# Kernel tuning notes

Measured on AMD Instinct MI355X. Metric: run time of the kernel, lower is better.

Reference implementation:

```python
import jax, jax.numpy as jnp
import numpy as np

T, B = 2048, 128
H = 128          # hidden_size
QH = 1024        # query_hidden_size
NF = 32          # num_convolution_filters
K = 31           # convolution_filter_size (odd, same padding)


def setup_inputs() -> dict:
    key = jax.random.key(0)
    ks = jax.random.split(key, 10)
    encoded_tokens = jax.random.normal(ks[0], (T, B, H), dtype=jnp.float32)
    tokens_mask = jax.random.randint(ks[1], (B, T), 0, 2).astype(jnp.bool_)
    query = jax.random.normal(ks[2], (1, B, QH), dtype=jnp.float32)
    cumulative_alignment = jax.random.uniform(ks[3], (B, T), dtype=jnp.float32)
    # parameters
    conv_w = jax.random.normal(ks[4], (NF, 1, K), dtype=jnp.float32) * 0.1   # Conv1d weight [out,in,k]
    conv_b = jnp.zeros((NF,), dtype=jnp.float32)
    Wq = jax.random.normal(ks[5], (H, QH), dtype=jnp.float32) * (1.0 / np.sqrt(QH))
    bq = jnp.zeros((H,), dtype=jnp.float32)
    Wa = jax.random.normal(ks[6], (H, NF), dtype=jnp.float32) * (1.0 / np.sqrt(NF))
    ba = jnp.zeros((H,), dtype=jnp.float32)
    score_w = jax.random.normal(ks[7], (H,), dtype=jnp.float32) * (1.0 / np.sqrt(H))  # xavier-ish
    score_b = jnp.zeros((H,), dtype=jnp.float32)
    return dict(encoded_tokens=encoded_tokens, tokens_mask=tokens_mask, query=query,
                cumulative_alignment=cumulative_alignment, conv_w=conv_w, conv_b=conv_b,
                Wq=Wq, bq=bq, Wa=Wa, ba=ba, score_w=score_w, score_b=score_b)


def reference(encoded_tokens, tokens_mask, query, cumulative_alignment,
              conv_w, conv_b, Wq, bq, Wa, ba, score_w, score_b):
    # location features: Conv1d over cumulative alignment, same padding
    loc = jax.lax.conv_general_dilated(
        cumulative_alignment[:, None, :], conv_w,
        window_strides=(1,), padding=[((K - 1) // 2, (K - 1) // 2)],
        dimension_numbers=('NCH', 'OIH', 'NCH'))  # [B, NF, T]
    loc = loc + conv_b[None, :, None]
    loc = jnp.transpose(loc, (2, 0, 1))                        # [T, B, NF]
    loc = jnp.einsum('tbf,hf->tbh', loc, Wa) + ba              # [T, B, H]
    q = jnp.einsum('obq,hq->obh', query, Wq) + bq              # [1, B, H]
    # additive score: tanh of fused elementwise sum, then project to scalar
    score = jnp.tanh(encoded_tokens + q + loc + score_b)       # [T, B, H]
    s = jnp.einsum('tbh,h->bt', score, score_w)                # [B, T]
    s = jnp.where(tokens_mask, -jnp.inf, s)
    alignment = jax.nn.softmax(s, axis=1)                      # [B, T]
    context = jnp.einsum('bt,tbh->bh', alignment, encoded_tokens)  # [B, H]
    cumulative_alignment = cumulative_alignment + alignment
    return context, cumulative_alignment, alignment
```

## Files before the change

### kernel.cpp

```cpp
#include <hip/hip_runtime.h>
#include <stdint.h>

#define T_DIM 2048
#define B_DIM 128
#define H_DIM 128
#define QH_DIM 1024
#define NF 32
#define KW 31
#define TB 128
#define NTILE (T_DIM / TB)
#define CPAD_ROW (T_DIM + 32)

#define PREP_NB 512
#define G_NB 8

#define NEG_INF (-__builtin_inff())

typedef float v2f __attribute__((ext_vector_type(2)));

__device__ __forceinline__ float fast_tanh(float x) {
    float e = __expf(2.0f * x);
    return 1.0f - 2.0f * __builtin_amdgcn_rcpf(1.0f + e);
}

template <int C>
__device__ __forceinline__ float dpp_add(float x) {
    int m = __builtin_amdgcn_update_dpp(0, __float_as_int(x), C, 0xf, 0xf, true);
    return x + __int_as_float(m);
}
__device__ __forceinline__ float wave_sum64(float x) {
    x = dpp_add<0x111>(x); x = dpp_add<0x112>(x); x = dpp_add<0x114>(x); x = dpp_add<0x118>(x);
    x = dpp_add<0x142>(x); x = dpp_add<0x143>(x);
    return __int_as_float(__builtin_amdgcn_readlane(__float_as_int(x), 63));
}

__global__ __launch_bounds__(512)
void kA_prep(const float* __restrict__ cum, const void* __restrict__ mask,
             float* __restrict__ cpad, float* __restrict__ mbias,
             const float* __restrict__ Wa, const float* __restrict__ conv_w,
             float* __restrict__ Gt,
             const float* __restrict__ query, const float* __restrict__ Wq,
             const float* __restrict__ bq, const float* __restrict__ conv_b,
             const float* __restrict__ ba, const float* __restrict__ score_b,
             float* __restrict__ qb) {
    const int bid = blockIdx.x;
    const int tid = threadIdx.x;

    if (bid < PREP_NB) {
        const int gid = bid * 512 + tid;
        const int b = gid >> 11, t = gid & 2047;
        const int l = tid & 63;
        uint32_t u = ((const uint32_t*)mask)[l];
        unsigned long long hi = __ballot(u > 1u);
        unsigned long long nf = __ballot(u != 0u && u != 0x3f800000u);
        int layout = (hi == 0ull) ? 0 : ((nf == 0ull) ? 2 : 1);
        bool m;
        if (layout == 0)      m = ((const int32_t*)mask)[gid] != 0;
        else if (layout == 1) m = ((const uint8_t*)mask)[gid] != 0;
        else                  m = ((const float*)mask)[gid] != 0.0f;
        mbias[gid] = m ? NEG_INF : 0.0f;
        cpad[b * CPAD_ROW + 16 + t] = cum[gid];
        if (t < 16) cpad[b * CPAD_ROW + t] = 0.0f;
        else if (t >= T_DIM - 16) cpad[b * CPAD_ROW + 32 + t] = 0.0f;
    } else if (bid < PREP_NB + G_NB) {
        const int gid = (bid - PREP_NB) * 512 + tid;
        if (gid < KW * H_DIM) {
            const int k = gid >> 7, h = gid & 127;
            float acc = 0.0f;
            #pragma unroll
            for (int f = 0; f < NF; ++f) acc = fmaf(Wa[h * NF + f], conv_w[f * KW + k], acc);
            Gt[gid] = acc;
        }
    } else {
        const int b = bid - (PREP_NB + G_NB);
        const int h = tid & 127, qtr = tid >> 7;
        __shared__ __align__(16) float qrow[QH_DIM];
        __shared__ float partial[512];
        for (int i = tid; i < QH_DIM; i += 512) qrow[i] = query[b * QH_DIM + i];
        __syncthreads();
        const float4* wq4 = (const float4*)(Wq + (size_t)h * QH_DIM + qtr * 256);
        const float4* q4 = (const float4*)(qrow + qtr * 256);
        float acc = 0.0f;
        #pragma unroll 4
        for (int j = 0; j < 64; ++j) {
            float4 w = wq4[j], q = q4[j];
            acc += w.x * q.x + w.y * q.y + w.z * q.z + w.w * q.w;
        }
        if (qtr == 0) {
            float cb = bq[h] + ba[h] + score_b[h];
            #pragma unroll
            for (int f = 0; f < NF; ++f) cb = fmaf(Wa[h * NF + f], conv_b[f], cb);
            acc += cb;
        }
        partial[tid] = acc;
        __syncthreads();
        if (tid < 128)
            qb[b * H_DIM + h] = partial[h] + partial[h + 128] + partial[h + 256] + partial[h + 384];
    }
}

__global__ __launch_bounds__(256, 4)
void k2_fused(const float* __restrict__ enc, const float* __restrict__ cpad,
              const float* __restrict__ mbias, const float* __restrict__ Gt,
              const float* __restrict__ qb, const float* __restrict__ score_w,
              float* __restrict__ s_out, float* __restrict__ o_part,
              float* __restrict__ ml_part) {
    const int b = blockIdx.x;
    const int tl = blockIdx.y;
    const int tid = threadIdx.x;
    const int l = tid & 63;
    const int wv = __builtin_amdgcn_readfirstlane(tid >> 6);
    const int tw0 = tl * TB + wv * 32;

    __shared__ float oc[4][H_DIM];
    __shared__ float mwl[4], lwl[4];

    v2f G[KW];
    #pragma unroll
    for (int k = 0; k < KW; ++k) G[k] = *(const v2f*)(Gt + k * H_DIM + 2 * l);

    const v2f base = *(const v2f*)(qb + b * H_DIM + 2 * l);
    const v2f w2 = *(const v2f*)(score_w + 2 * l);
    const float* crow = cpad + b * CPAD_ROW;
    const float* mrow = mbias + b * T_DIM;

    float m_w = NEG_INF, l_w = 0.0f;
    v2f o = {0.0f, 0.0f};
    float sv = 0.0f;

    #pragma unroll
    for (int c = 0; c < 4; ++c) {
        const int tb = tw0 + c * 8;

        float sc[38];
        #pragma unroll
        for (int j = 0; j < 38; ++j) sc[j] = crow[tb + 1 + j];

        v2f ee[8];
        #pragma unroll
        for (int it = 0; it < 8; ++it)
            ee[it] = *(const v2f*)(enc + ((size_t)(tb + it) * B_DIM + b) * H_DIM + 2 * l);

        float su[8];
        #pragma unroll
        for (int it = 0; it < 8; ++it) {
            v2f acc = base;
            #pragma unroll
            for (int k = 0; k < KW; ++k)
                acc = __builtin_elementwise_fma(G[k], (v2f){sc[it + k], sc[it + k]}, acc);
            const v2f a2 = acc + ee[it];
            float p = w2.x * fast_tanh(a2.x) + w2.y * fast_tanh(a2.y);
            su[it] = wave_sum64(p) + mrow[tb + it];
        }

        #pragma unroll
        for (int it = 0; it < 8; ++it) sv = (l == c * 8 + it) ? su[it] : sv;

        float m8 = su[0];
        #pragma unroll
        for (int it = 1; it < 8; ++it) m8 = fmaxf(m8, su[it]);
        const float m_new = fmaxf(m_w, m8);
        const float m_use = (m_new == NEG_INF) ? 0.0f : m_new;
        const float alpha = __expf(m_w - m_use);
        float lsum = 0.0f;
        v2f osum = {0.0f, 0.0f};
        #pragma unroll
        for (int it = 0; it < 8; ++it) {
            const float e = __expf(su[it] - m_use);
            lsum += e;
            osum = __builtin_elementwise_fma((v2f){e, e}, ee[it], osum);
        }
        l_w = fmaf(l_w, alpha, lsum);
        o = __builtin_elementwise_fma(o, (v2f){alpha, alpha}, osum);
        m_w = m_new;
    }

    if (l < 32) s_out[b * T_DIM + tw0 + l] = sv;

    oc[wv][2 * l] = o.x;
    oc[wv][2 * l + 1] = o.y;
    if (l == 0) { mwl[wv] = m_w; lwl[wv] = l_w; }
    __syncthreads();
    if (tid < H_DIM) {
        const float mb = fmaxf(fmaxf(mwl[0], mwl[1]), fmaxf(mwl[2], mwl[3]));
        const float mu = (mb == NEG_INF) ? 0.0f : mb;
        const float b0 = __expf(mwl[0] - mu), b1 = __expf(mwl[1] - mu);
        const float b2 = __expf(mwl[2] - mu), b3 = __expf(mwl[3] - mu);
        const float ov = oc[0][tid] * b0 + oc[1][tid] * b1 + oc[2][tid] * b2 + oc[3][tid] * b3;
        const int tbase = b * NTILE + tl;
        o_part[tbase * H_DIM + tid] = ov;
        if (tid == 0) {
            ml_part[tbase * 2] = mb;
            ml_part[tbase * 2 + 1] = lwl[0] * b0 + lwl[1] * b1 + lwl[2] * b2 + lwl[3] * b3;
        }
    }
}

__global__ __launch_bounds__(256)
void k5_final(float* __restrict__ s_align, const float* __restrict__ cum_in,
              float* __restrict__ cum_out, const float* __restrict__ o_part,
              const float* __restrict__ ml_part, float* __restrict__ ctx) {
    const int b = blockIdx.x, seg = blockIdx.y, tid = threadIdx.x;
    __shared__ float sm[NTILE], sl[NTILE], sb[NTILE];
    if (tid < NTILE) {
        sm[tid] = ml_part[(b * NTILE + tid) * 2];
        sl[tid] = ml_part[(b * NTILE + tid) * 2 + 1];
    }
    __syncthreads();
    float M = sm[0];
    #pragma unroll
    for (int i = 1; i < NTILE; ++i) M = fmaxf(M, sm[i]);
    const float M_use = (M == NEG_INF) ? 0.0f : M;
    if (tid < NTILE) sb[tid] = __expf(sm[tid] - M_use);
    __syncthreads();
    float L = 0.0f;
    #pragma unroll
    for (int i = 0; i < NTILE; ++i) L = fmaf(sl[i], sb[i], L);
    const float invL = 1.0f / L;
    if (seg == 0 && tid < H_DIM) {
        float ov = 0.0f;
        #pragma unroll
        for (int i = 0; i < NTILE; ++i)
            ov = fmaf(o_part[(b * NTILE + i) * H_DIM + tid], sb[i], ov);
        ctx[b * H_DIM + tid] = ov * invL;
    }
    #pragma unroll
    for (int j = 0; j < 2; ++j) {
        const int idx = b * T_DIM + seg * 512 + tid + j * 256;
        const float a = __expf(s_align[idx] - M_use) * invL;
        s_align[idx] = a;
        cum_out[idx] = cum_in[idx] + a;
    }
}

extern "C" void kernel_launch(void* const* d_in, const int* in_sizes, int n_in,
                              void* d_out, int out_size, void* d_ws, size_t ws_size,
                              hipStream_t stream) {
    const float* enc     = (const float*)d_in[0];
    const void*  mask    = d_in[1];
    const float* query   = (const float*)d_in[2];
    const float* cum     = (const float*)d_in[3];
    const float* conv_w  = (const float*)d_in[4];
    const float* conv_b  = (const float*)d_in[5];
    const float* Wq      = (const float*)d_in[6];
    const float* bq      = (const float*)d_in[7];
    const float* Wa      = (const float*)d_in[8];
    const float* ba      = (const float*)d_in[9];
    const float* score_w = (const float*)d_in[10];
    const float* score_b = (const float*)d_in[11];

    float* ctx_out   = (float*)d_out;
    float* cum_out   = ctx_out + B_DIM * H_DIM;
    float* align_out = cum_out + B_DIM * T_DIM;

    float* Gt     = (float*)d_ws;
    float* qb     = Gt + 4096;
    float* o_part = qb + B_DIM * H_DIM;
    float* ml     = o_part + B_DIM * NTILE * H_DIM;
    float* cpad   = ml + 8192;
    float* mb     = cpad + B_DIM * CPAD_ROW;

    kA_prep<<<PREP_NB + G_NB + B_DIM, 512, 0, stream>>>(
        cum, mask, cpad, mb, Wa, conv_w, Gt,
        query, Wq, bq, conv_b, ba, score_b, qb);
    k2_fused<<<dim3(B_DIM, NTILE), 256, 0, stream>>>(enc, cpad, mb, Gt, qb, score_w,
                                                     align_out, o_part, ml);
    k5_final<<<dim3(B_DIM, 4), 256, 0, stream>>>(align_out, cum, cum_out, o_part, ml, ctx_out);
}
```

Measured before the change: 233.5 us.

## Split query projection across more blocks and double-buffer encoder loads

The query projection in the prep kernel is split into four segment blocks per batch row, each writing a partial result. The fused kernel now sums the four partials when it forms its base vector. The fused kernel also prefetches the next chunk of encoder rows into a double buffer while the current chunk is computed, which is meant to hide global load latency. Launch bounds drop from 4 to 3 blocks per SM to make room for the extra registers, which trades occupancy for software pipelining.

```diff
diff --git a/kernel.cpp b/kernel.cpp
--- a/kernel.cpp
+++ b/kernel.cpp
@@ -13,6 +13,7 @@
 
 #define PREP_NB 512
 #define G_NB 8
+#define QB_SEG 4
 
 #define NEG_INF (-__builtin_inff())
 
@@ -42,7 +43,7 @@
              const float* __restrict__ query, const float* __restrict__ Wq,
              const float* __restrict__ bq, const float* __restrict__ conv_b,
              const float* __restrict__ ba, const float* __restrict__ score_b,
-             float* __restrict__ qb) {
+             float* __restrict__ qb_part) {
     const int bid = blockIdx.x;
     const int tid = threadIdx.x;
 
@@ -72,37 +73,40 @@
             Gt[gid] = acc;
         }
     } else {
-        const int b = bid - (PREP_NB + G_NB);
-        const int h = tid & 127, qtr = tid >> 7;
-        __shared__ __align__(16) float qrow[QH_DIM];
+        const int qbid = bid - (PREP_NB + G_NB);
+        const int b = qbid >> 2, seg = qbid & 3;
+        const int h = tid & 127, sub = tid >> 7;
+        __shared__ __align__(16) float qrow[256];
         __shared__ float partial[512];
-        for (int i = tid; i < QH_DIM; i += 512) qrow[i] = query[b * QH_DIM + i];
+        if (tid < 256) qrow[tid] = query[b * QH_DIM + seg * 256 + tid];
         __syncthreads();
-        const float4* wq4 = (const float4*)(Wq + (size_t)h * QH_DIM + qtr * 256);
-        const float4* q4 = (const float4*)(qrow + qtr * 256);
+        const float4* wq4 = (const float4*)(Wq + (size_t)h * QH_DIM + seg * 256 + sub * 64);
+        const float4* q4 = (const float4*)(qrow + sub * 64);
         float acc = 0.0f;
-        #pragma unroll 4
-        for (int j = 0; j < 64; ++j) {
+        #pragma unroll
+        for (int j = 0; j < 16; ++j) {
             float4 w = wq4[j], q = q4[j];
             acc += w.x * q.x + w.y * q.y + w.z * q.z + w.w * q.w;
         }
-        if (qtr == 0) {
-            float cb = bq[h] + ba[h] + score_b[h];
-            #pragma unroll
-            for (int f = 0; f < NF; ++f) cb = fmaf(Wa[h * NF + f], conv_b[f], cb);
-            acc += cb;
-        }
         partial[tid] = acc;
         __syncthreads();
-        if (tid < 128)
-            qb[b * H_DIM + h] = partial[h] + partial[h + 128] + partial[h + 256] + partial[h + 384];
-    }
-}
-
-__global__ __launch_bounds__(256, 4)
+        if (tid < 128) {
+            float r = partial[h] + partial[h + 128] + partial[h + 256] + partial[h + 384];
+            if (seg == 0) {
+                float cb = bq[h] + ba[h] + score_b[h];
+                #pragma unroll
+                for (int f = 0; f < NF; ++f) cb = fmaf(Wa[h * NF + f], conv_b[f], cb);
+                r += cb;
+            }
+            qb_part[(seg * B_DIM + b) * H_DIM + h] = r;
+        }
+    }
+}
+
+__global__ __launch_bounds__(256, 3)
 void k2_fused(const float* __restrict__ enc, const float* __restrict__ cpad,
               const float* __restrict__ mbias, const float* __restrict__ Gt,
-              const float* __restrict__ qb, const float* __restrict__ score_w,
+              const float* __restrict__ qb_part, const float* __restrict__ score_w,
               float* __restrict__ s_out, float* __restrict__ o_part,
               float* __restrict__ ml_part) {
     const int b = blockIdx.x;
@@ -119,27 +123,40 @@
     #pragma unroll
     for (int k = 0; k < KW; ++k) G[k] = *(const v2f*)(Gt + k * H_DIM + 2 * l);
 
-    const v2f base = *(const v2f*)(qb + b * H_DIM + 2 * l);
+    const float* qp = qb_part + b * H_DIM + 2 * l;
+    v2f base = *(const v2f*)(qp);
+    base += *(const v2f*)(qp + B_DIM * H_DIM);
+    base += *(const v2f*)(qp + 2 * B_DIM * H_DIM);
+    base += *(const v2f*)(qp + 3 * B_DIM * H_DIM);
+
     const v2f w2 = *(const v2f*)(score_w + 2 * l);
     const float* crow = cpad + b * CPAD_ROW;
     const float* mrow = mbias + b * T_DIM;
+    const float* erow = enc + ((size_t)tw0 * B_DIM + b) * H_DIM + 2 * l;
 
     float m_w = NEG_INF, l_w = 0.0f;
     v2f o = {0.0f, 0.0f};
     float sv = 0.0f;
 
+    v2f eeb[2][8];
+    #pragma unroll
+    for (int it = 0; it < 8; ++it)
+        eeb[0][it] = *(const v2f*)(erow + (size_t)it * B_DIM * H_DIM);
+
     #pragma unroll
     for (int c = 0; c < 4; ++c) {
         const int tb = tw0 + c * 8;
 
+        if (c < 3) {
+            #pragma unroll
+            for (int it = 0; it < 8; ++it)
+                eeb[(c + 1) & 1][it] =
+                    *(const v2f*)(erow + (size_t)(c * 8 + 8 + it) * B_DIM * H_DIM);
+        }
+
         float sc[38];
         #pragma unroll
         for (int j = 0; j < 38; ++j) sc[j] = crow[tb + 1 + j];
-
-        v2f ee[8];
-        #pragma unroll
-        for (int it = 0; it < 8; ++it)
-            ee[it] = *(const v2f*)(enc + ((size_t)(tb + it) * B_DIM + b) * H_DIM + 2 * l);
 
         float su[8];
         #pragma unroll
@@ -148,7 +165,7 @@
             #pragma unroll
             for (int k = 0; k < KW; ++k)
                 acc = __builtin_elementwise_fma(G[k], (v2f){sc[it + k], sc[it + k]}, acc);
-            const v2f a2 = acc + ee[it];
+            const v2f a2 = acc + eeb[c & 1][it];
             float p = w2.x * fast_tanh(a2.x) + w2.y * fast_tanh(a2.y);
             su[it] = wave_sum64(p) + mrow[tb + it];
         }
@@ -168,7 +185,7 @@
         for (int it = 0; it < 8; ++it) {
             const float e = __expf(su[it] - m_use);
             lsum += e;
-            osum = __builtin_elementwise_fma((v2f){e, e}, ee[it], osum);
+            osum = __builtin_elementwise_fma((v2f){e, e}, eeb[c & 1][it], osum);
         }
         l_w = fmaf(l_w, alpha, lsum);
         o = __builtin_elementwise_fma(o, (v2f){alpha, alpha}, osum);
@@ -253,17 +270,17 @@
     float* cum_out   = ctx_out + B_DIM * H_DIM;
     float* align_out = cum_out + B_DIM * T_DIM;
 
-    float* Gt     = (float*)d_ws;
-    float* qb     = Gt + 4096;
-    float* o_part = qb + B_DIM * H_DIM;
-    float* ml     = o_part + B_DIM * NTILE * H_DIM;
-    float* cpad   = ml + 8192;
-    float* mb     = cpad + B_DIM * CPAD_ROW;
-
-    kA_prep<<<PREP_NB + G_NB + B_DIM, 512, 0, stream>>>(
+    float* Gt      = (float*)d_ws;
+    float* qb_part = Gt + 4096;
+    float* o_part  = qb_part + 4 * B_DIM * H_DIM;
+    float* ml      = o_part + B_DIM * NTILE * H_DIM;
+    float* cpad    = ml + 8192;
+    float* mb      = cpad + B_DIM * CPAD_ROW;
+
+    kA_prep<<<PREP_NB + G_NB + QB_SEG * B_DIM, 512, 0, stream>>>(
         cum, mask, cpad, mb, Wa, conv_w, Gt,
-        query, Wq, bq, conv_b, ba, score_b, qb);
-    k2_fused<<<dim3(B_DIM, NTILE), 256, 0, stream>>>(enc, cpad, mb, Gt, qb, score_w,
+        query, Wq, bq, conv_b, ba, score_b, qb_part);
+    k2_fused<<<dim3(B_DIM, NTILE), 256, 0, stream>>>(enc, cpad, mb, Gt, qb_part, score_w,
                                                      align_out, o_part, ml);
     k5_final<<<dim3(B_DIM, 4), 256, 0, stream>>>(align_out, cum, cum_out, o_part, ml, ctx_out);
 }
```

New measurement: 236.0 us. About the same (+1.1%).
